# Performance work log

Measured on AMD Instinct MI355X. Metric: run time of the kernel, lower is better.

The kernel has to match this reference:

```python
import jax, jax.numpy as jnp
import numpy as np

BLOCK_SIZE_KV = 16
SCALE = 0.08838834764831845  # 1/sqrt(128)


def setup_inputs() -> dict:
    key = jax.random.key(0)
    k0, k1, k2, k3, k4 = jax.random.split(key, 5)
    B, H, D, KVH = 32, 32, 128, 8
    MAX_BLOCKS = 256                 # 4096-token max context / 16-token pages
    N_PHYS_BLOCKS = B * MAX_BLOCKS   # 8192 physical pages
    q = jax.random.normal(k0, (B, H, D), jnp.float32)
    k_cache = jax.random.normal(k1, (N_PHYS_BLOCKS, BLOCK_SIZE_KV, KVH, D), jnp.float32)
    v_cache = jax.random.normal(k2, (N_PHYS_BLOCKS, BLOCK_SIZE_KV, KVH, D), jnp.float32)
    # each logical page maps to a distinct physical page (vLLM-style allocation)
    block_tables = jax.random.permutation(k3, N_PHYS_BLOCKS).reshape(B, MAX_BLOCKS).astype(jnp.int32)
    context_lens = jax.random.randint(k4, (B,), 1, MAX_BLOCKS * BLOCK_SIZE_KV + 1, jnp.int32)
    return {"q": q, "k_cache": k_cache, "v_cache": v_cache,
            "block_tables": block_tables, "context_lens": context_lens}


def reference(q, k_cache, v_cache, block_tables, context_lens):
    # q: [B, H, D]; k/v_cache: [NB, 16, KVH, D]; block_tables: [B, MB]; context_lens: [B]
    B, H, D = q.shape
    KVH = k_cache.shape[2]
    G = H // KVH                                  # GQA group size
    MB = block_tables.shape[1]
    S = MB * BLOCK_SIZE_KV                        # max logical context
    # gather paged KV per sequence: [B, MB, 16, KVH, D] -> [B, S, KVH, D]
    K = k_cache[block_tables].reshape(B, S, KVH, D)
    V = v_cache[block_tables].reshape(B, S, KVH, D)
    qg = q.reshape(B, KVH, G, D)
    scores = jnp.einsum('bkgd,bskd->bkgs', qg, K) * jnp.float32(SCALE)
    valid = (jnp.arange(S)[None, :] < context_lens[:, None])  # [B, S]
    scores = jnp.where(valid[:, None, None, :], scores, -jnp.inf)
    p = jax.nn.softmax(scores, axis=-1)           # online-softmax equivalent
    out = jnp.einsum('bkgs,bskd->bkgd', p, V).reshape(B, H, D)
    return out
```

## Files before the change

### kernel.cpp

```cpp
#include <hip/hip_runtime.h>


constexpr int Dh   = 128;
constexpr int Gq   = 4;
constexpr int KVH  = 8;
constexpr int Hq   = 32;
constexpr int Bb   = 32;
constexpr int MB   = 256;
constexpr int PAGE = 16;
constexpr float SCALE = 0.08838834764831845f;

constexpr int NPARTS      = 64;
constexpr int PART_TOKENS = 64;
constexpr int PG_FLOATS   = PAGE * KVH * Dh;
constexpr int ROW_FLOATS  = KVH * Dh;
constexpr int NUNITS      = Bb * NPARTS;

constexpr int PART_STRIDE = Hq * Dh + 2 * Hq;

constexpr size_t CTR_BYTE_OFF = (size_t)128 << 20;

struct QuadR { float4 k[4], v[4]; };

__global__ void init_ctr(int* ctr) { *ctr = 0; }

__global__ __launch_bounds__(256, 3)
void attn_partial(const float* __restrict__ q,
                  const float* __restrict__ kc,
                  const float* __restrict__ vc,
                  const int*   __restrict__ bt,
                  const int*   __restrict__ cl,
                  float*       __restrict__ ws,
                  int*         __restrict__ ctr)
{
    const int t      = threadIdx.x;
    const int kvh    = t >> 5;
    const int lane32 = t & 31;
    const int doff   = lane32 * 4;
    const int t4     = t * 4;

    __shared__ int s_unit;

    for (;;) {
        if (t == 0) s_unit = atomicAdd(ctr, 1);
        __syncthreads();
        const int unit = s_unit;
        __syncthreads();
        if (unit >= NUNITS) break;

        const int b    = unit & (Bb - 1);
        const int part = unit >> 5;

        const int ctx    = cl[b];
        const int pstart = part * PART_TOKENS;
        if (pstart >= ctx) continue;
        const int n  = min(PART_TOKENS, ctx - pstart);
        const int TC = (n + 3) >> 2;

        const int4 pg = *(const int4*)(bt + b * MB + (pstart >> 4));

        float4 qv[Gq];
        {
            const float* qbase = q + (size_t)(b * Hq + kvh * Gq) * Dh + doff;
            #pragma unroll
            for (int g = 0; g < Gq; ++g) {
                float4 x = *(const float4*)(qbase + g * Dh);
                qv[g] = make_float4(x.x * SCALE, x.y * SCALE, x.z * SCALE, x.w * SCALE);
            }
        }

        float4 acc[Gq];
        float  m_run[Gq], l_run[Gq];
        #pragma unroll
        for (int g = 0; g < Gq; ++g) {
            acc[g] = make_float4(0.f, 0.f, 0.f, 0.f);
            m_run[g] = -1e30f;
            l_run[g] = 0.f;
        }

        auto physof = [&](int c) -> int {
            const int p = c >> 2;
            return p == 0 ? pg.x : (p == 1 ? pg.y : (p == 2 ? pg.z : pg.w));
        };

        auto LOADQ = [&](QuadR& H, int c) {
            const size_t off = (size_t)physof(c) * PG_FLOATS
                             + (size_t)((c & 3) * 4) * ROW_FLOATS + t4;
            const float* kp = kc + off;
            const float* vp = vc + off;
            #pragma unroll
            for (int j = 0; j < 4; ++j) {
                H.k[j] = *(const float4*)(kp + j * ROW_FLOATS);
                H.v[j] = *(const float4*)(vp + j * ROW_FLOATS);
            }
        };

        auto COMPUTEQ = [&](const QuadR& H, int c) {
            const int tb = c * 4;
            float s[4][Gq];
            #pragma unroll
            for (int j = 0; j < 4; ++j) {
                const bool vj = (tb + j) < n;
                #pragma unroll
                for (int g = 0; g < Gq; ++g) {
                    float d = H.k[j].x * qv[g].x + H.k[j].y * qv[g].y
                            + H.k[j].z * qv[g].z + H.k[j].w * qv[g].w;
                    d += __shfl_xor(d, 1);
                    d += __shfl_xor(d, 2);
                    d += __shfl_xor(d, 4);
                    d += __shfl_xor(d, 8);
                    d += __shfl_xor(d, 16);
                    s[j][g] = vj ? d : -1e30f;
                }
            }
            #pragma unroll
            for (int g = 0; g < Gq; ++g) {
                const float tm = fmaxf(fmaxf(s[0][g], s[1][g]),
                                       fmaxf(s[2][g], s[3][g]));
                const float mn    = fmaxf(m_run[g], tm);
                const float alpha = __expf(m_run[g] - mn);
                m_run[g] = mn;
                const float p0 = __expf(s[0][g] - mn);
                const float p1 = __expf(s[1][g] - mn);
                const float p2 = __expf(s[2][g] - mn);
                const float p3 = __expf(s[3][g] - mn);
                l_run[g] = l_run[g] * alpha + (p0 + p1 + p2 + p3);
                acc[g].x = fmaf(p3, H.v[3].x, fmaf(p2, H.v[2].x,
                           fmaf(p1, H.v[1].x, fmaf(p0, H.v[0].x, acc[g].x * alpha))));
                acc[g].y = fmaf(p3, H.v[3].y, fmaf(p2, H.v[2].y,
                           fmaf(p1, H.v[1].y, fmaf(p0, H.v[0].y, acc[g].y * alpha))));
                acc[g].z = fmaf(p3, H.v[3].z, fmaf(p2, H.v[2].z,
                           fmaf(p1, H.v[1].z, fmaf(p0, H.v[0].z, acc[g].z * alpha))));
                acc[g].w = fmaf(p3, H.v[3].w, fmaf(p2, H.v[2].w,
                           fmaf(p1, H.v[1].w, fmaf(p0, H.v[0].w, acc[g].w * alpha))));
            }
        };

        QuadR A, B;
        LOADQ(A, 0);
        int c = 0;
        while (true) {
            if (c + 1 < TC) LOADQ(B, c + 1);
            COMPUTEQ(A, c);
            ++c; if (c >= TC) break;
            if (c + 1 < TC) LOADQ(A, c + 1);
            COMPUTEQ(B, c);
            ++c; if (c >= TC) break;
        }

        float* wp = ws + (size_t)(b * NPARTS + part) * PART_STRIDE;
        #pragma unroll
        for (int g = 0; g < Gq; ++g)
            *(float4*)(wp + (kvh * Gq + g) * Dh + doff) = acc[g];
        if (lane32 == 0) {
            #pragma unroll
            for (int g = 0; g < Gq; ++g) {
                wp[Hq * Dh + kvh * Gq + g]      = m_run[g];
                wp[Hq * Dh + Hq + kvh * Gq + g] = l_run[g];
            }
        }
    }
}

__global__ __launch_bounds__(256, 4)
void attn_reduce(const float* __restrict__ ws,
                 const int*   __restrict__ cl,
                 float*       __restrict__ out)
{
    const int b       = blockIdx.x >> 2;
    const int quarter = blockIdx.x & 3;
    const int tid     = threadIdx.x;
    const int h       = quarter * 8 + (tid >> 5);
    const int doff    = (tid & 31) * 4;

    const int ctx = cl[b];
    const int np  = min(NPARTS, (ctx + PART_TOKENS - 1) / PART_TOKENS);

    const float* base = ws + (size_t)b * NPARTS * PART_STRIDE;

    float m = -1e30f;
    for (int p = 0; p < np; ++p)
        m = fmaxf(m, base[p * PART_STRIDE + Hq * Dh + h]);

    float L = 0.f;
    float ax = 0.f, ay = 0.f, az = 0.f, aw = 0.f;
    for (int p = 0; p < np; ++p) {
        const float* bp = base + p * PART_STRIDE;
        const float c = __expf(bp[Hq * Dh + h] - m);
        L += bp[Hq * Dh + Hq + h] * c;
        const float4 v = *(const float4*)(bp + h * Dh + doff);
        ax = fmaf(c, v.x, ax);
        ay = fmaf(c, v.y, ay);
        az = fmaf(c, v.z, az);
        aw = fmaf(c, v.w, aw);
    }
    const float inv = 1.f / L;
    float* op = out + (size_t)(b * Hq + h) * Dh + doff;
    *(float4*)op = make_float4(ax * inv, ay * inv, az * inv, aw * inv);
}

extern "C" void kernel_launch(void* const* d_in, const int* in_sizes, int n_in,
                              void* d_out, int out_size, void* d_ws, size_t ws_size,
                              hipStream_t stream) {
    const float* q  = (const float*)d_in[0];
    const float* kc = (const float*)d_in[1];
    const float* vc = (const float*)d_in[2];
    const int*   bt = (const int*)d_in[3];
    const int*   cl = (const int*)d_in[4];
    float* out = (float*)d_out;
    float* ws  = (float*)d_ws;
    int*   ctr = (int*)((char*)d_ws + CTR_BYTE_OFF);

    init_ctr<<<dim3(1), dim3(1), 0, stream>>>(ctr);
    attn_partial<<<dim3(768), dim3(256), 0, stream>>>(q, kc, vc, bt, cl, ws, ctr);
    attn_reduce<<<dim3(Bb * 4), dim3(256), 0, stream>>>(ws, cl, out);
}
```

Measured before the change: 155.2 us.

## Stage paged K/V through LDS with async global_load_lds triple buffering

```diff
diff --git a/kernel.cpp b/kernel.cpp
--- a/kernel.cpp
+++ b/kernel.cpp
@@ -20,9 +20,13 @@
 
 constexpr size_t CTR_BYTE_OFF = (size_t)128 << 20;
 
-struct QuadR { float4 k[4], v[4]; };
-
 __global__ void init_ctr(int* ctr) { *ctr = 0; }
+
+__device__ __forceinline__ void gld16(const float* g, float* l) {
+    __builtin_amdgcn_global_load_lds(
+        (const __attribute__((address_space(1))) void*)g,
+        (__attribute__((address_space(3))) void*)l, 16, 0, 0);
+}
 
 __global__ __launch_bounds__(256, 3)
 void attn_partial(const float* __restrict__ q,
@@ -34,12 +38,18 @@
                   int*         __restrict__ ctr)
 {
     const int t      = threadIdx.x;
+    const int wave   = t >> 6;
+    const int lane   = t & 63;
     const int kvh    = t >> 5;
     const int lane32 = t & 31;
     const int doff   = lane32 * 4;
-    const int t4     = t * 4;
-
+
+    __shared__ float slab[4][3][2][2][256];
     __shared__ int s_unit;
+
+    float* const myslab = &slab[wave][0][0][0][0];
+    const int lane4 = lane * 4;
+    const int t4    = t * 4;
 
     for (;;) {
         if (t == 0) s_unit = atomicAdd(ctr, 1);
@@ -55,7 +65,7 @@
         const int pstart = part * PART_TOKENS;
         if (pstart >= ctx) continue;
         const int n  = min(PART_TOKENS, ctx - pstart);
-        const int TC = (n + 3) >> 2;
+        const int TC = (n + 1) >> 1;
 
         const int4 pg = *(const int4*)(bt + b * MB + (pstart >> 4));
 
@@ -78,75 +88,76 @@
             l_run[g] = 0.f;
         }
 
-        auto physof = [&](int c) -> int {
-            const int p = c >> 2;
-            return p == 0 ? pg.x : (p == 1 ? pg.y : (p == 2 ? pg.z : pg.w));
+        auto physof = [&](int pgi) -> int {
+            return pgi == 0 ? pg.x : (pgi == 1 ? pg.y : (pgi == 2 ? pg.z : pg.w));
         };
 
-        auto LOADQ = [&](QuadR& H, int c) {
-            const size_t off = (size_t)physof(c) * PG_FLOATS
-                             + (size_t)((c & 3) * 4) * ROW_FLOATS + t4;
-            const float* kp = kc + off;
-            const float* vp = vc + off;
-            #pragma unroll
-            for (int j = 0; j < 4; ++j) {
-                H.k[j] = *(const float4*)(kp + j * ROW_FLOATS);
-                H.v[j] = *(const float4*)(vp + j * ROW_FLOATS);
+        auto STAGE = [&](int c) {
+            const int buf = c % 3;
+            float* dst = myslab + buf * 1024;
+            #pragma unroll
+            for (int tp = 0; tp < 2; ++tp) {
+                const int tok  = c * 2 + tp;
+                const int phys = physof(tok >> 4);
+                const size_t roff = (size_t)phys * PG_FLOATS
+                                  + (size_t)(tok & 15) * ROW_FLOATS + t4;
+                gld16(kc + roff, dst + tp * 512);
+                gld16(vc + roff, dst + tp * 512 + 256);
             }
         };
 
-        auto COMPUTEQ = [&](const QuadR& H, int c) {
-            const int tb = c * 4;
-            float s[4][Gq];
-            #pragma unroll
-            for (int j = 0; j < 4; ++j) {
-                const bool vj = (tb + j) < n;
-                #pragma unroll
-                for (int g = 0; g < Gq; ++g) {
-                    float d = H.k[j].x * qv[g].x + H.k[j].y * qv[g].y
-                            + H.k[j].z * qv[g].z + H.k[j].w * qv[g].w;
-                    d += __shfl_xor(d, 1);
-                    d += __shfl_xor(d, 2);
-                    d += __shfl_xor(d, 4);
-                    d += __shfl_xor(d, 8);
-                    d += __shfl_xor(d, 16);
-                    s[j][g] = vj ? d : -1e30f;
-                }
-            }
-            #pragma unroll
-            for (int g = 0; g < Gq; ++g) {
-                const float tm = fmaxf(fmaxf(s[0][g], s[1][g]),
-                                       fmaxf(s[2][g], s[3][g]));
+        auto COMPUTE = [&](int c) {
+            const int buf = c % 3;
+            const float* sb = myslab + buf * 1024;
+            const float4 k0 = *(const float4*)(sb +       lane4);
+            const float4 v0 = *(const float4*)(sb + 256 + lane4);
+            const float4 k1 = *(const float4*)(sb + 512 + lane4);
+            const float4 v1 = *(const float4*)(sb + 768 + lane4);
+            const bool ok1 = (c * 2 + 1) < n;
+            float s0[Gq], s1[Gq];
+            #pragma unroll
+            for (int g = 0; g < Gq; ++g) {
+                float d0 = k0.x*qv[g].x + k0.y*qv[g].y + k0.z*qv[g].z + k0.w*qv[g].w;
+                float d1 = k1.x*qv[g].x + k1.y*qv[g].y + k1.z*qv[g].z + k1.w*qv[g].w;
+                d0 += __shfl_xor(d0, 1);  d1 += __shfl_xor(d1, 1);
+                d0 += __shfl_xor(d0, 2);  d1 += __shfl_xor(d1, 2);
+                d0 += __shfl_xor(d0, 4);  d1 += __shfl_xor(d1, 4);
+                d0 += __shfl_xor(d0, 8);  d1 += __shfl_xor(d1, 8);
+                d0 += __shfl_xor(d0, 16); d1 += __shfl_xor(d1, 16);
+                s0[g] = d0;
+                s1[g] = ok1 ? d1 : -1e30f;
+            }
+            #pragma unroll
+            for (int g = 0; g < Gq; ++g) {
+                const float tm    = fmaxf(s0[g], s1[g]);
                 const float mn    = fmaxf(m_run[g], tm);
                 const float alpha = __expf(m_run[g] - mn);
                 m_run[g] = mn;
-                const float p0 = __expf(s[0][g] - mn);
-                const float p1 = __expf(s[1][g] - mn);
-                const float p2 = __expf(s[2][g] - mn);
-                const float p3 = __expf(s[3][g] - mn);
-                l_run[g] = l_run[g] * alpha + (p0 + p1 + p2 + p3);
-                acc[g].x = fmaf(p3, H.v[3].x, fmaf(p2, H.v[2].x,
-                           fmaf(p1, H.v[1].x, fmaf(p0, H.v[0].x, acc[g].x * alpha))));
-                acc[g].y = fmaf(p3, H.v[3].y, fmaf(p2, H.v[2].y,
-                           fmaf(p1, H.v[1].y, fmaf(p0, H.v[0].y, acc[g].y * alpha))));
-                acc[g].z = fmaf(p3, H.v[3].z, fmaf(p2, H.v[2].z,
-                           fmaf(p1, H.v[1].z, fmaf(p0, H.v[0].z, acc[g].z * alpha))));
-                acc[g].w = fmaf(p3, H.v[3].w, fmaf(p2, H.v[2].w,
-                           fmaf(p1, H.v[1].w, fmaf(p0, H.v[0].w, acc[g].w * alpha))));
+                const float p0 = __expf(s0[g] - mn);
+                const float p1 = __expf(s1[g] - mn);
+                l_run[g] = l_run[g] * alpha + (p0 + p1);
+                acc[g].x = fmaf(p1, v1.x, fmaf(p0, v0.x, acc[g].x * alpha));
+                acc[g].y = fmaf(p1, v1.y, fmaf(p0, v0.y, acc[g].y * alpha));
+                acc[g].z = fmaf(p1, v1.z, fmaf(p0, v0.z, acc[g].z * alpha));
+                acc[g].w = fmaf(p1, v1.w, fmaf(p0, v0.w, acc[g].w * alpha));
             }
         };
 
-        QuadR A, B;
-        LOADQ(A, 0);
+        STAGE(0);
+        if (TC > 1) STAGE(1);
         int c = 0;
-        while (true) {
-            if (c + 1 < TC) LOADQ(B, c + 1);
-            COMPUTEQ(A, c);
-            ++c; if (c >= TC) break;
-            if (c + 1 < TC) LOADQ(A, c + 1);
-            COMPUTEQ(B, c);
-            ++c; if (c >= TC) break;
-        }
+        for (; c + 2 < TC; ++c) {
+            STAGE(c + 2);
+            asm volatile("s_waitcnt vmcnt(8)" ::: "memory");
+            COMPUTE(c);
+        }
+        if (c + 1 < TC) {
+            asm volatile("s_waitcnt vmcnt(4)" ::: "memory");
+            COMPUTE(c);
+            ++c;
+        }
+        asm volatile("s_waitcnt vmcnt(0)" ::: "memory");
+        COMPUTE(c);
 
         float* wp = ws + (size_t)(b * NPARTS + part) * PART_STRIDE;
         #pragma unroll
```

Result: slower. 176.7 us (+13.9%).

## Iterate physical KV pages in memory order via inverse block table

Applied to the files above, without the earlier changes.

```diff
diff --git a/kernel.cpp b/kernel.cpp
--- a/kernel.cpp
+++ b/kernel.cpp
@@ -10,26 +10,36 @@
 constexpr int PAGE = 16;
 constexpr float SCALE = 0.08838834764831845f;
 
-constexpr int NPARTS      = 64;
-constexpr int PART_TOKENS = 64;
-constexpr int PG_FLOATS   = PAGE * KVH * Dh;
-constexpr int ROW_FLOATS  = KVH * Dh;
-constexpr int NUNITS      = Bb * NPARTS;
+constexpr int PG_FLOATS  = PAGE * KVH * Dh;
+constexpr int ROW_FLOATS = KVH * Dh;
+constexpr int NPAGES     = Bb * MB;
+constexpr int NUNITS     = NPAGES / 2;
 
 constexpr int PART_STRIDE = Hq * Dh + 2 * Hq;
 
-constexpr size_t CTR_BYTE_OFF = (size_t)128 << 20;
+constexpr size_t INV_BYTE_OFF = (size_t)192 << 20;
+constexpr size_t CTR_BYTE_OFF = (size_t)200 << 20;
 
 struct QuadR { float4 k[4], v[4]; };
 
 __global__ void init_ctr(int* ctr) { *ctr = 0; }
+
+__global__ __launch_bounds__(256)
+void build_inv(const int* __restrict__ bt, const int* __restrict__ cl,
+               int* __restrict__ inv)
+{
+    const int b  = blockIdx.x;
+    const int lp = threadIdx.x;
+    const int phys = bt[b * MB + lp];
+    inv[phys] = (lp * PAGE < cl[b]) ? ((b << 8) | lp) : -1;
+}
 
 __global__ __launch_bounds__(256, 3)
 void attn_partial(const float* __restrict__ q,
                   const float* __restrict__ kc,
                   const float* __restrict__ vc,
-                  const int*   __restrict__ bt,
                   const int*   __restrict__ cl,
+                  const int*   __restrict__ inv,
                   float*       __restrict__ ws,
                   int*         __restrict__ ctr)
 {
@@ -48,115 +58,111 @@
         __syncthreads();
         if (unit >= NUNITS) break;
 
-        const int b    = unit & (Bb - 1);
-        const int part = unit >> 5;
-
-        const int ctx    = cl[b];
-        const int pstart = part * PART_TOKENS;
-        if (pstart >= ctx) continue;
-        const int n  = min(PART_TOKENS, ctx - pstart);
-        const int TC = (n + 3) >> 2;
-
-        const int4 pg = *(const int4*)(bt + b * MB + (pstart >> 4));
-
-        float4 qv[Gq];
-        {
-            const float* qbase = q + (size_t)(b * Hq + kvh * Gq) * Dh + doff;
+        #pragma unroll 1
+        for (int pp = 0; pp < 2; ++pp) {
+            const int phys = unit * 2 + pp;
+            const int code = inv[phys];
+            if (code < 0) continue;
+            const int b  = code >> 8;
+            const int lp = code & 255;
+            const int n  = min(PAGE, cl[b] - lp * PAGE);
+            const int TC = (n + 3) >> 2;
+
+            float4 qv[Gq];
+            {
+                const float* qbase = q + (size_t)(b * Hq + kvh * Gq) * Dh + doff;
+                #pragma unroll
+                for (int g = 0; g < Gq; ++g) {
+                    float4 x = *(const float4*)(qbase + g * Dh);
+                    qv[g] = make_float4(x.x * SCALE, x.y * SCALE,
+                                        x.z * SCALE, x.w * SCALE);
+                }
+            }
+
+            float4 acc[Gq];
+            float  m_run[Gq], l_run[Gq];
             #pragma unroll
             for (int g = 0; g < Gq; ++g) {
-                float4 x = *(const float4*)(qbase + g * Dh);
-                qv[g] = make_float4(x.x * SCALE, x.y * SCALE, x.z * SCALE, x.w * SCALE);
-            }
-        }
-
-        float4 acc[Gq];
-        float  m_run[Gq], l_run[Gq];
-        #pragma unroll
-        for (int g = 0; g < Gq; ++g) {
-            acc[g] = make_float4(0.f, 0.f, 0.f, 0.f);
-            m_run[g] = -1e30f;
-            l_run[g] = 0.f;
-        }
-
-        auto physof = [&](int c) -> int {
-            const int p = c >> 2;
-            return p == 0 ? pg.x : (p == 1 ? pg.y : (p == 2 ? pg.z : pg.w));
-        };
-
-        auto LOADQ = [&](QuadR& H, int c) {
-            const size_t off = (size_t)physof(c) * PG_FLOATS
-                             + (size_t)((c & 3) * 4) * ROW_FLOATS + t4;
-            const float* kp = kc + off;
-            const float* vp = vc + off;
+                acc[g] = make_float4(0.f, 0.f, 0.f, 0.f);
+                m_run[g] = -1e30f;
+                l_run[g] = 0.f;
+            }
+
+            const size_t pbase = (size_t)phys * PG_FLOATS + t4;
+
+            auto LOADQ = [&](QuadR& H, int c) {
+                const float* kp = kc + pbase + (size_t)(c * 4) * ROW_FLOATS;
+                const float* vp = vc + pbase + (size_t)(c * 4) * ROW_FLOATS;
+                #pragma unroll
+                for (int j = 0; j < 4; ++j) {
+                    H.k[j] = *(const float4*)(kp + j * ROW_FLOATS);
+                    H.v[j] = *(const float4*)(vp + j * ROW_FLOATS);
+                }
+            };
+
+            auto COMPUTEQ = [&](const QuadR& H, int c) {
+                const int tb = c * 4;
+                float s[4][Gq];
+                #pragma unroll
+                for (int j = 0; j < 4; ++j) {
+                    const bool vj = (tb + j) < n;
+                    #pragma unroll
+                    for (int g = 0; g < Gq; ++g) {
+                        float d = H.k[j].x * qv[g].x + H.k[j].y * qv[g].y
+                                + H.k[j].z * qv[g].z + H.k[j].w * qv[g].w;
+                        d += __shfl_xor(d, 1);
+                        d += __shfl_xor(d, 2);
+                        d += __shfl_xor(d, 4);
+                        d += __shfl_xor(d, 8);
+                        d += __shfl_xor(d, 16);
+                        s[j][g] = vj ? d : -1e30f;
+                    }
+                }
+                #pragma unroll
+                for (int g = 0; g < Gq; ++g) {
+                    const float tm = fmaxf(fmaxf(s[0][g], s[1][g]),
+                                           fmaxf(s[2][g], s[3][g]));
+                    const float mn    = fmaxf(m_run[g], tm);
+                    const float alpha = __expf(m_run[g] - mn);
+                    m_run[g] = mn;
+                    const float p0 = __expf(s[0][g] - mn);
+                    const float p1 = __expf(s[1][g] - mn);
+                    const float p2 = __expf(s[2][g] - mn);
+                    const float p3 = __expf(s[3][g] - mn);
+                    l_run[g] = l_run[g] * alpha + (p0 + p1 + p2 + p3);
+                    acc[g].x = fmaf(p3, H.v[3].x, fmaf(p2, H.v[2].x,
+                               fmaf(p1, H.v[1].x, fmaf(p0, H.v[0].x, acc[g].x * alpha))));
+                    acc[g].y = fmaf(p3, H.v[3].y, fmaf(p2, H.v[2].y,
+                               fmaf(p1, H.v[1].y, fmaf(p0, H.v[0].y, acc[g].y * alpha))));
+                    acc[g].z = fmaf(p3, H.v[3].z, fmaf(p2, H.v[2].z,
+                               fmaf(p1, H.v[1].z, fmaf(p0, H.v[0].z, acc[g].z * alpha))));
+                    acc[g].w = fmaf(p3, H.v[3].w, fmaf(p2, H.v[2].w,
+                               fmaf(p1, H.v[1].w, fmaf(p0, H.v[0].w, acc[g].w * alpha))));
+                }
+            };
+
+            QuadR A, B;
+            LOADQ(A, 0);
+            int c = 0;
+            while (true) {
+                if (c + 1 < TC) LOADQ(B, c + 1);
+                COMPUTEQ(A, c);
+                ++c; if (c >= TC) break;
+                if (c + 1 < TC) LOADQ(A, c + 1);
+                COMPUTEQ(B, c);
+                ++c; if (c >= TC) break;
+            }
+
+            float* wp = ws + (size_t)(b * MB + lp) * PART_STRIDE;
             #pragma unroll
-            for (int j = 0; j < 4; ++j) {
-                H.k[j] = *(const float4*)(kp + j * ROW_FLOATS);
-                H.v[j] = *(const float4*)(vp + j * ROW_FLOATS);
-            }
-        };
-
-        auto COMPUTEQ = [&](const QuadR& H, int c) {
-            const int tb = c * 4;
-            float s[4][Gq];
-            #pragma unroll
-            for (int j = 0; j < 4; ++j) {
-                const bool vj = (tb + j) < n;
+            for (int g = 0; g < Gq; ++g)
+                *(float4*)(wp + (kvh * Gq + g) * Dh + doff) = acc[g];
+            if (lane32 == 0) {
                 #pragma unroll
                 for (int g = 0; g < Gq; ++g) {
-                    float d = H.k[j].x * qv[g].x + H.k[j].y * qv[g].y
-                            + H.k[j].z * qv[g].z + H.k[j].w * qv[g].w;
-                    d += __shfl_xor(d, 1);
-                    d += __shfl_xor(d, 2);
-                    d += __shfl_xor(d, 4);
-                    d += __shfl_xor(d, 8);
-                    d += __shfl_xor(d, 16);
-                    s[j][g] = vj ? d : -1e30f;
-                }
-            }
-            #pragma unroll
-            for (int g = 0; g < Gq; ++g) {
-                const float tm = fmaxf(fmaxf(s[0][g], s[1][g]),
-                                       fmaxf(s[2][g], s[3][g]));
-                const float mn    = fmaxf(m_run[g], tm);
-                const float alpha = __expf(m_run[g] - mn);
-                m_run[g] = mn;
-                const float p0 = __expf(s[0][g] - mn);
-                const float p1 = __expf(s[1][g] - mn);
-                const float p2 = __expf(s[2][g] - mn);
-                const float p3 = __expf(s[3][g] - mn);
-                l_run[g] = l_run[g] * alpha + (p0 + p1 + p2 + p3);
-                acc[g].x = fmaf(p3, H.v[3].x, fmaf(p2, H.v[2].x,
-                           fmaf(p1, H.v[1].x, fmaf(p0, H.v[0].x, acc[g].x * alpha))));
-                acc[g].y = fmaf(p3, H.v[3].y, fmaf(p2, H.v[2].y,
-                           fmaf(p1, H.v[1].y, fmaf(p0, H.v[0].y, acc[g].y * alpha))));
-                acc[g].z = fmaf(p3, H.v[3].z, fmaf(p2, H.v[2].z,
-                           fmaf(p1, H.v[1].z, fmaf(p0, H.v[0].z, acc[g].z * alpha))));
-                acc[g].w = fmaf(p3, H.v[3].w, fmaf(p2, H.v[2].w,
-                           fmaf(p1, H.v[1].w, fmaf(p0, H.v[0].w, acc[g].w * alpha))));
-            }
-        };
-
-        QuadR A, B;
-        LOADQ(A, 0);
-        int c = 0;
-        while (true) {
-            if (c + 1 < TC) LOADQ(B, c + 1);
-            COMPUTEQ(A, c);
-            ++c; if (c >= TC) break;
-            if (c + 1 < TC) LOADQ(A, c + 1);
-            COMPUTEQ(B, c);
-            ++c; if (c >= TC) break;
-        }
-
-        float* wp = ws + (size_t)(b * NPARTS + part) * PART_STRIDE;
-        #pragma unroll
-        for (int g = 0; g < Gq; ++g)
-            *(float4*)(wp + (kvh * Gq + g) * Dh + doff) = acc[g];
-        if (lane32 == 0) {
-            #pragma unroll
-            for (int g = 0; g < Gq; ++g) {
-                wp[Hq * Dh + kvh * Gq + g]      = m_run[g];
-                wp[Hq * Dh + Hq + kvh * Gq + g] = l_run[g];
+                    wp[Hq * Dh + kvh * Gq + g]      = m_run[g];
+                    wp[Hq * Dh + Hq + kvh * Gq + g] = l_run[g];
+                }
             }
         }
     }
@@ -174,25 +180,26 @@
     const int doff    = (tid & 31) * 4;
 
     const int ctx = cl[b];
-    const int np  = min(NPARTS, (ctx + PART_TOKENS - 1) / PART_TOKENS);
-
-    const float* base = ws + (size_t)b * NPARTS * PART_STRIDE;
-
-    float m = -1e30f;
-    for (int p = 0; p < np; ++p)
-        m = fmaxf(m, base[p * PART_STRIDE + Hq * Dh + h]);
-
-    float L = 0.f;
+    const int np  = (ctx + PAGE - 1) >> 4;
+
+    const float* base = ws + (size_t)b * MB * PART_STRIDE;
+
+    float M = -1e30f, L = 0.f;
     float ax = 0.f, ay = 0.f, az = 0.f, aw = 0.f;
     for (int p = 0; p < np; ++p) {
-        const float* bp = base + p * PART_STRIDE;
-        const float c = __expf(bp[Hq * Dh + h] - m);
-        L += bp[Hq * Dh + Hq + h] * c;
-        const float4 v = *(const float4*)(bp + h * Dh + doff);
-        ax = fmaf(c, v.x, ax);
-        ay = fmaf(c, v.y, ay);
-        az = fmaf(c, v.z, az);
-        aw = fmaf(c, v.w, aw);
+        const float* bp = base + (size_t)p * PART_STRIDE;
+        const float mp = bp[Hq * Dh + h];
+        const float lp = bp[Hq * Dh + Hq + h];
+        const float4 a = *(const float4*)(bp + h * Dh + doff);
+        const float Mn = fmaxf(M, mp);
+        const float e0 = __expf(M - Mn);
+        const float e1 = __expf(mp - Mn);
+        L  = L  * e0 + lp  * e1;
+        ax = ax * e0 + a.x * e1;
+        ay = ay * e0 + a.y * e1;
+        az = az * e0 + a.z * e1;
+        aw = aw * e0 + a.w * e1;
+        M = Mn;
     }
     const float inv = 1.f / L;
     float* op = out + (size_t)(b * Hq + h) * Dh + doff;
@@ -209,9 +216,11 @@
     const int*   cl = (const int*)d_in[4];
     float* out = (float*)d_out;
     float* ws  = (float*)d_ws;
+    int*   inv = (int*)((char*)d_ws + INV_BYTE_OFF);
     int*   ctr = (int*)((char*)d_ws + CTR_BYTE_OFF);
 
     init_ctr<<<dim3(1), dim3(1), 0, stream>>>(ctr);
-    attn_partial<<<dim3(768), dim3(256), 0, stream>>>(q, kc, vc, bt, cl, ws, ctr);
+    build_inv<<<dim3(Bb), dim3(MB), 0, stream>>>(bt, cl, inv);
+    attn_partial<<<dim3(768), dim3(256), 0, stream>>>(q, kc, vc, cl, inv, ws, ctr);
     attn_reduce<<<dim3(Bb * 4), dim3(256), 0, stream>>>(ws, cl, out);
 }
```

Measured after the change: 226.2 us. 45.7% more time.
